# Kernel tuning notes

Measured on AMD Instinct MI355X. Metric: run time of the kernel, lower is better.

Reference implementation:

```python
import jax, jax.numpy as jnp
import numpy as np

B, C_LEN, Q_LEN, D = 8, 2048, 512, 1024


def setup_inputs() -> dict:
    key = jax.random.key(0)
    ks = jax.random.split(key, 10)
    scale = 1.0 / np.sqrt(D)
    return {
        "c": jax.random.normal(ks[0], (B, C_LEN, D), dtype=jnp.float32),
        "q": jax.random.normal(ks[1], (B, Q_LEN, D), dtype=jnp.float32),
        "w_cq": jax.random.normal(ks[2], (D,), dtype=jnp.float32) * scale,
        "b_cq": jax.random.normal(ks[3], (), dtype=jnp.float32) * scale,
        "w_c": jax.random.normal(ks[4], (D,), dtype=jnp.float32) * scale,
        "b_c": jax.random.normal(ks[5], (), dtype=jnp.float32) * scale,
        "w_q": jax.random.normal(ks[6], (D,), dtype=jnp.float32) * scale,
        "b_q": jax.random.normal(ks[7], (), dtype=jnp.float32) * scale,
        "W_l": jax.random.normal(ks[8], (D, 4 * D), dtype=jnp.float32) * (1.0 / np.sqrt(4 * D)),
        "b_l": jax.random.normal(ks[9], (D,), dtype=jnp.float32) * (1.0 / np.sqrt(4 * D)),
    }


def reference(c, q, w_cq, b_cq, w_c, b_c, w_q, b_q, W_l, b_l):
    # trilinear term: the original loops over q positions computing
    # att_weight_cq(c * q_i); since that Linear is rank-1, this is one einsum.
    cq = jnp.einsum('bcd,bqd,d->bcq', c, q, w_cq) + b_cq        # [B, C, Q]
    s = (c @ w_c + b_c)[:, :, None] + (q @ w_q + b_q)[:, None, :] + cq
    a = jax.nn.softmax(s, axis=2)                               # c2q attention
    c2q_att = jnp.einsum('bcq,bqd->bcd', a, q)                  # [B, C, D]
    b_att = jax.nn.softmax(jnp.max(s, axis=2), axis=1)          # [B, C]
    q2c_att = jnp.einsum('bc,bcd->bd', b_att, c)[:, None, :]    # [B, 1, D]
    x = jnp.concatenate([c, c2q_att, c * c2q_att, c * q2c_att], axis=-1)
    z = x @ W_l.T + b_l                                         # [B, C, D]
    return z
```

## Files before the change

kernel.cpp:

```cpp
#include <hip/hip_runtime.h>

typedef unsigned short u16;
typedef __attribute__((ext_vector_type(4))) float floatx4;
typedef __attribute__((ext_vector_type(4))) unsigned short u16x4;
typedef __attribute__((ext_vector_type(8))) short short8;
typedef __attribute__((ext_vector_type(8))) __bf16 bf16x8;

#define B_SZ 8
#define C_LEN 2048
#define Q_LEN 512
#define D_DIM 1024
#define K4 (4 * D_DIM)

static __device__ __forceinline__ u16 f2bf(float f) {
    union { float f; unsigned int u; } v; v.f = f;
    unsigned int r = v.u + 0x7FFFu + ((v.u >> 16) & 1u);
    return (u16)(r >> 16);
}
static __device__ __forceinline__ float bf2f(u16 h) {
    union { unsigned int u; float f; } v; v.u = ((unsigned int)h) << 16;
    return v.f;
}

static __device__ __forceinline__ void async16(const void* g, void* l) {
    __builtin_amdgcn_global_load_lds(
        (const __attribute__((address_space(1))) unsigned int*)g,
        (__attribute__((address_space(3))) unsigned int*)(unsigned int)(unsigned long long)l,
        16, 0, 0);
}

__global__ __launch_bounds__(256) void prep_kernel(
    const float* __restrict__ c, const float* __restrict__ q,
    const float* __restrict__ w_cq, const float* __restrict__ w_c, const float* __restrict__ w_q,
    u16* __restrict__ cbf, u16* __restrict__ qwbf, u16* __restrict__ qT,
    float* __restrict__ rowterm, float* __restrict__ colterm, float* __restrict__ q2c) {
    int blk = blockIdx.x;
    int tid = threadIdx.x;
    if (blk < 4096) {
        int row = blk * 4 + (tid >> 6);
        int lane = tid & 63;
        const float* src = c + (size_t)row * D_DIM;
        u16* dst = cbf + (size_t)row * D_DIM;
        float s = 0.f;
        #pragma unroll
        for (int j = 0; j < 4; ++j) {
            int idx = j * 256 + lane * 4;
            floatx4 a = *(const floatx4*)(src + idx);
            floatx4 w = *(const floatx4*)(w_c + idx);
            s += a[0]*w[0] + a[1]*w[1] + a[2]*w[2] + a[3]*w[3];
            u16x4 o;
            #pragma unroll
            for (int e = 0; e < 4; ++e) o[e] = f2bf(a[e]);
            *(u16x4*)(dst + idx) = o;
        }
        for (int off = 32; off; off >>= 1) s += __shfl_down(s, off);
        if (lane == 0) rowterm[row] = s;
    } else if (blk < 5120) {
        int row = (blk - 4096) * 4 + (tid >> 6);
        int lane = tid & 63;
        const float* src = q + (size_t)row * D_DIM;
        u16* dst = qwbf + (size_t)row * D_DIM;
        float s = 0.f;
        #pragma unroll
        for (int j = 0; j < 4; ++j) {
            int idx = j * 256 + lane * 4;
            floatx4 a  = *(const floatx4*)(src + idx);
            floatx4 wc = *(const floatx4*)(w_cq + idx);
            floatx4 wq = *(const floatx4*)(w_q + idx);
            s += a[0]*wq[0] + a[1]*wq[1] + a[2]*wq[2] + a[3]*wq[3];
            u16x4 o;
            #pragma unroll
            for (int e = 0; e < 4; ++e) o[e] = f2bf(a[e] * wc[e]);
            *(u16x4*)(dst + idx) = o;
        }
        for (int off = 32; off; off >>= 1) s += __shfl_down(s, off);
        if (lane == 0) colterm[row] = s;
    } else if (blk < 9216) {
        __shared__ float tile[32][33];
        int t = blk - 5120;
        int q0 = (t & 15) * 32;
        int d0 = ((t >> 4) & 31) * 32;
        int b = t >> 9;
        int tx = tid & 31, ty = tid >> 5;
        const float* qb = q + (size_t)b * Q_LEN * D_DIM;
        #pragma unroll
        for (int j = 0; j < 4; ++j) {
            int row = ty + j * 8;
            tile[row][tx] = qb[(size_t)(q0 + row) * D_DIM + d0 + tx];
        }
        __syncthreads();
        u16* qTb = qT + (size_t)b * D_DIM * Q_LEN;
        #pragma unroll
        for (int j = 0; j < 4; ++j) {
            int row = ty + j * 8;
            qTb[(size_t)(d0 + row) * Q_LEN + q0 + tx] = f2bf(tile[tx][row]);
        }
    } else {
        int i = (blk - 9216) * 256 + tid;
        q2c[i] = 0.0f;
    }
}

__global__ __launch_bounds__(256) void wmerge_all(const float* __restrict__ W, const float* __restrict__ q2c,
                                                  u16* __restrict__ Wm, u16* __restrict__ Wbf) {
    int n = blockIdx.x;
    int k = threadIdx.x * 4;
    const float* wr = W + (size_t)n * K4;
    floatx4 w1 = *(const floatx4*)(wr + k);
    floatx4 w4 = *(const floatx4*)(wr + 3072 + k);
    #pragma unroll
    for (int p = 0; p < 2; ++p) {
        int kk = p * 1024 + k;
        floatx4 v = *(const floatx4*)(wr + 1024 + kk);
        u16x4 o;
        #pragma unroll
        for (int e = 0; e < 4; ++e) o[e] = f2bf(v[e]);
        *(u16x4*)(Wbf + (size_t)n * 2048 + kk) = o;
    }
    #pragma unroll
    for (int b = 0; b < 8; ++b) {
        floatx4 g = *(const floatx4*)(q2c + (size_t)b * D_DIM + k);
        u16x4 o;
        #pragma unroll
        for (int e = 0; e < 4; ++e) o[e] = f2bf(w1[e] + w4[e] * g[e]);
        *(u16x4*)(Wm + (size_t)b * 1048576 + (size_t)n * 1024 + k) = o;
    }
}

template<int MODE>
__global__ __launch_bounds__(256) void gemm_async(
    const u16* __restrict__ A0, const u16* __restrict__ A1, const u16* __restrict__ A2,
    const u16* __restrict__ B0, const u16* __restrict__ B1,
    float* __restrict__ of, u16* __restrict__ ob, const float* __restrict__ bias) {
    constexpr int NSEC = (MODE == 2) ? 3 : 1;
    constexpr int KSEC = (MODE == 1) ? 512 : 1024;
    constexpr int LDO  = (MODE == 0) ? 512 : 1024;
    constexpr int NTILES = (MODE == 0) ? 4 : 8;
    __shared__ u16 As[128 * 64];
    __shared__ u16 Bs[128 * 64];
    const int tid  = threadIdx.x;
    const int lane = tid & 63;
    const int wave = tid >> 6;
    const int lin  = blockIdx.x;
    const int b    = lin & 7;
    const int rem  = lin >> 3;
    const int n0   = (rem % NTILES) * 128;
    const int m0   = (rem / NTILES) * 128;

    const u16* Aarr[NSEC];
    const u16* Barr[NSEC];
    int lda_[NSEC], ldb_[NSEC];
    if constexpr (MODE == 0) {
        Aarr[0] = A0 + (size_t)b * C_LEN * D_DIM; lda_[0] = 1024;
        Barr[0] = B0 + (size_t)b * Q_LEN * D_DIM; ldb_[0] = 1024;
    } else if constexpr (MODE == 1) {
        Aarr[0] = A0 + (size_t)b * C_LEN * Q_LEN; lda_[0] = 512;
        Barr[0] = B0 + (size_t)b * D_DIM * Q_LEN; ldb_[0] = 512;
    } else {
        Aarr[0] = A0 + (size_t)b * C_LEN * D_DIM;  lda_[0] = 1024;
        Barr[0] = B0 + (size_t)b * D_DIM * D_DIM;  ldb_[0] = 1024;
        Aarr[1] = A1 + (size_t)b * C_LEN * 2048;        lda_[1] = 2048;
        Barr[1] = B1;                                   ldb_[1] = 2048;
        Aarr[2] = A1 + (size_t)b * C_LEN * 2048 + 1024; lda_[2] = 2048;
        Barr[2] = B1 + 1024;                            ldb_[2] = 2048;
    }

    const int srow = lane >> 3;
    const int ssc  = ((lane & 7) ^ srow) * 8;

    floatx4 acc[4][4];
    #pragma unroll
    for (int i = 0; i < 4; ++i)
        #pragma unroll
        for (int j = 0; j < 4; ++j)
            acc[i][j] = (floatx4)(0.0f);

    const int wrow = (wave >> 1) * 64;
    const int wcol = (wave & 1) * 64;
    const int quad = lane >> 4;
    const int lrow = lane & 15;
    const int sw7  = lane & 7;

    #pragma unroll
    for (int sec = 0; sec < NSEC; ++sec) {
        const u16* __restrict__ Ab = Aarr[sec];
        const u16* __restrict__ Bb = Barr[sec];
        const int LA = lda_[sec];
        const int LB = ldb_[sec];
        for (int k0 = 0; k0 < KSEC; k0 += 64) {
            #pragma unroll
            for (int cc = 0; cc < 4; ++cc) {
                int ch = wave * 4 + cc;
                int rr = ch * 8 + srow;
                async16(Ab + (size_t)(m0 + rr) * LA + k0 + ssc, &As[ch * 512]);
            }
            #pragma unroll
            for (int cc = 0; cc < 4; ++cc) {
                int ch = wave * 4 + cc;
                int rr = ch * 8 + srow;
                async16(Bb + (size_t)(n0 + rr) * LB + k0 + ssc, &Bs[ch * 512]);
            }
            __syncthreads();
            #pragma unroll
            for (int h = 0; h < 2; ++h) {
                const int pc = ((h * 4 + quad) ^ sw7) * 8;
                bf16x8 af[4], bfr[4];
                #pragma unroll
                for (int i = 0; i < 4; ++i)
                    af[i] = __builtin_bit_cast(bf16x8, *(const short8*)&As[(wrow + i*16 + lrow) * 64 + pc]);
                #pragma unroll
                for (int j = 0; j < 4; ++j)
                    bfr[j] = __builtin_bit_cast(bf16x8, *(const short8*)&Bs[(wcol + j*16 + lrow) * 64 + pc]);
                #pragma unroll
                for (int i = 0; i < 4; ++i)
                    #pragma unroll
                    for (int j = 0; j < 4; ++j)
                        acc[i][j] = __builtin_amdgcn_mfma_f32_16x16x32_bf16(af[i], bfr[j], acc[i][j], 0, 0, 0);
            }
            __syncthreads();
        }
    }

    float* ofb = nullptr; u16* ccb = nullptr; const u16* cbr = nullptr;
    if (MODE == 0)      ofb = of + (size_t)b * C_LEN * Q_LEN;
    else if (MODE == 1) { ccb = ob + (size_t)b * C_LEN * 2048; cbr = A1 + (size_t)b * C_LEN * D_DIM; }
    else                ofb = of + (size_t)b * C_LEN * D_DIM;
    #pragma unroll
    for (int i = 0; i < 4; ++i) {
        #pragma unroll
        for (int j = 0; j < 4; ++j) {
            #pragma unroll
            for (int e = 0; e < 4; ++e) {
                int gm = m0 + wrow + i * 16 + quad * 4 + e;
                int gn = n0 + wcol + j * 16 + lrow;
                float v = acc[i][j][e];
                if (MODE == 0)      ofb[(size_t)gm * LDO + gn] = v;
                else if (MODE == 1) {
                    u16 p = f2bf(v);
                    float cv = bf2f(cbr[(size_t)gm * 1024 + gn]);
                    ccb[(size_t)gm * 2048 + gn]        = p;
                    ccb[(size_t)gm * 2048 + 1024 + gn] = f2bf(cv * bf2f(p));
                }
                else                ofb[(size_t)gm * LDO + gn] = v + bias[gn];
            }
        }
    }
}

__global__ void softmax_kernel(const float* __restrict__ S, const float* __restrict__ colterm,
                               u16* __restrict__ P, float* __restrict__ mbuf) {
    int row = blockIdx.x * 4 + (threadIdx.x >> 6);
    int lane = threadIdx.x & 63;
    int b = row >> 11;
    const float* sp = S + (size_t)row * Q_LEN;
    const float* cp = colterm + (size_t)b * Q_LEN;
    float v[8];
    float m = -1e30f;
    #pragma unroll
    for (int j = 0; j < 8; ++j) {
        int idx = j * 64 + lane;
        v[j] = sp[idx] + cp[idx];
        m = fmaxf(m, v[j]);
    }
    for (int off = 32; off; off >>= 1) m = fmaxf(m, __shfl_xor(m, off));
    float s = 0.f;
    #pragma unroll
    for (int j = 0; j < 8; ++j) { v[j] = __expf(v[j] - m); s += v[j]; }
    for (int off = 32; off; off >>= 1) s += __shfl_xor(s, off);
    float inv = 1.0f / s;
    u16* pp = P + (size_t)row * Q_LEN;
    #pragma unroll
    for (int j = 0; j < 8; ++j) pp[j * 64 + lane] = f2bf(v[j] * inv);
    if (lane == 0) mbuf[row] = m;
}

__global__ __launch_bounds__(256) void batt_kernel(const float* __restrict__ mbuf,
                                                   const float* __restrict__ rowterm,
                                                   float* __restrict__ batt) {
    __shared__ float red[8];
    int b = blockIdx.x;
    int tid = threadIdx.x;
    const float* mb = mbuf + (size_t)b * C_LEN;
    const float* rt = rowterm + (size_t)b * C_LEN;
    float v[8];
    float m = -1e30f;
    #pragma unroll
    for (int j = 0; j < 8; ++j) { int idx = j * 256 + tid; v[j] = mb[idx] + rt[idx]; m = fmaxf(m, v[j]); }
    for (int off = 32; off; off >>= 1) m = fmaxf(m, __shfl_xor(m, off));
    int wave = tid >> 6, lane = tid & 63;
    if (lane == 0) red[wave] = m;
    __syncthreads();
    m = fmaxf(fmaxf(red[0], red[1]), fmaxf(red[2], red[3]));
    float s = 0.f;
    #pragma unroll
    for (int j = 0; j < 8; ++j) { v[j] = __expf(v[j] - m); s += v[j]; }
    for (int off = 32; off; off >>= 1) s += __shfl_xor(s, off);
    if (lane == 0) red[4 + wave] = s;
    __syncthreads();
    s = red[4] + red[5] + red[6] + red[7];
    float inv = 1.0f / s;
    float* bb = batt + (size_t)b * C_LEN;
    #pragma unroll
    for (int j = 0; j < 8; ++j) bb[j * 256 + tid] = v[j] * inv;
}

__global__ __launch_bounds__(256) void q2c_kernel(const float* __restrict__ batt,
                                                  const u16* __restrict__ cbf,
                                                  float* __restrict__ q2c) {
    int d  = blockIdx.x * 256 + threadIdx.x;
    int b  = blockIdx.y;
    int c0 = blockIdx.z * 256;
    const u16* cb = cbf + ((size_t)b * C_LEN + c0) * D_DIM + d;
    const float* bb = batt + (size_t)b * C_LEN + c0;
    float s = 0.f;
    #pragma unroll 4
    for (int i = 0; i < 256; ++i) s += bb[i] * bf2f(cb[(size_t)i * D_DIM]);
    atomicAdd(&q2c[(size_t)b * D_DIM + d], s);
}

extern "C" void kernel_launch(void* const* d_in, const int* in_sizes, int n_in,
                              void* d_out, int out_size, void* d_ws, size_t ws_size,
                              hipStream_t stream) {
    const float* c   = (const float*)d_in[0];
    const float* q   = (const float*)d_in[1];
    const float* wcq = (const float*)d_in[2];
    const float* w_c = (const float*)d_in[4];
    const float* w_q = (const float*)d_in[6];
    const float* W_l = (const float*)d_in[8];
    const float* b_l = (const float*)d_in[9];
    float* out = (float*)d_out;

    char* ws = (char*)d_ws;
    u16*   cbf     = (u16*)ws;
    float* S       = (float*)(ws + 33554432);
    u16*   CC      = (u16*)(ws + 33554432);
    u16*   qwbf    = (u16*)(ws + 67108864);
    u16*   P       = (u16*)(ws + 100663296);
    u16*   Wm      = (u16*)(ws + 100663296);
    u16*   qT      = (u16*)(ws + 117440512);
    u16*   Wbf     = (u16*)(ws + 117440512);
    float* rowterm = (float*)(ws + 125829120);
    float* colterm = (float*)(ws + 125894656);
    float* mbuf    = (float*)(ws + 125911040);
    float* batt    = (float*)(ws + 125976576);
    float* q2c     = (float*)(ws + 126042112);

    prep_kernel<<<dim3(9248), dim3(256), 0, stream>>>(c, q, wcq, w_c, w_q,
                                                      cbf, qwbf, qT, rowterm, colterm, q2c);
    gemm_async<0><<<dim3(512), dim3(256), 0, stream>>>(cbf, nullptr, nullptr, qwbf, nullptr, S, nullptr, nullptr);
    softmax_kernel<<<dim3(4096), dim3(256), 0, stream>>>(S, colterm, P, mbuf);
    batt_kernel<<<dim3(8), dim3(256), 0, stream>>>(mbuf, rowterm, batt);
    q2c_kernel<<<dim3(4, 8, 8), dim3(256), 0, stream>>>(batt, cbf, q2c);
    gemm_async<1><<<dim3(1024), dim3(256), 0, stream>>>(P, cbf, nullptr, qT, nullptr, nullptr, CC, nullptr);
    wmerge_all<<<dim3(1024), dim3(256), 0, stream>>>(W_l, q2c, Wm, Wbf);
    gemm_async<2><<<dim3(1024), dim3(256), 0, stream>>>(cbf, CC, nullptr, Wm, Wbf, out, nullptr, b_l);
}
```

Before: 364.8 us.

## Reassociate c2q projection through W2 so final GEMM consumes P directly

The c2q_att @ W2^T term is rewritten as P @ (q @ W2^T), so a new small GEMM (mode 3) computes W2q = W2·q^T per batch and the final GEMM uses P (K=512) in place of the c2q block (K=1024). The mode-1 GEMM now only writes the c*c2q product instead of both c2q and the product. This shrinks the final GEMM's K, its A reads and mode-1's writes, at the cost of one extra GEMM that converts fp32 q to bf16 on the fly with synchronous loads. The reassociation also changes where bf16 rounding happens.

```diff
diff --git a/kernel.cpp b/kernel.cpp
--- a/kernel.cpp
+++ b/kernel.cpp
@@ -130,12 +130,12 @@
 template<int MODE>
 __global__ __launch_bounds__(256) void gemm_async(
     const u16* __restrict__ A0, const u16* __restrict__ A1, const u16* __restrict__ A2,
-    const u16* __restrict__ B0, const u16* __restrict__ B1,
+    const u16* __restrict__ B0, const u16* __restrict__ B1, const u16* __restrict__ B2,
+    const float* __restrict__ fB,
     float* __restrict__ of, u16* __restrict__ ob, const float* __restrict__ bias) {
     constexpr int NSEC = (MODE == 2) ? 3 : 1;
-    constexpr int KSEC = (MODE == 1) ? 512 : 1024;
-    constexpr int LDO  = (MODE == 0) ? 512 : 1024;
-    constexpr int NTILES = (MODE == 0) ? 4 : 8;
+    constexpr int LDO  = (MODE == 0 || MODE == 3) ? 512 : 1024;
+    constexpr int NTILES = (MODE == 0 || MODE == 3) ? 4 : 8;
     __shared__ u16 As[128 * 64];
     __shared__ u16 Bs[128 * 64];
     const int tid  = threadIdx.x;
@@ -149,20 +149,25 @@
 
     const u16* Aarr[NSEC];
     const u16* Barr[NSEC];
-    int lda_[NSEC], ldb_[NSEC];
+    const float* Bf = nullptr;
+    int lda_[NSEC], ldb_[NSEC], ks_[NSEC];
     if constexpr (MODE == 0) {
         Aarr[0] = A0 + (size_t)b * C_LEN * D_DIM; lda_[0] = 1024;
-        Barr[0] = B0 + (size_t)b * Q_LEN * D_DIM; ldb_[0] = 1024;
+        Barr[0] = B0 + (size_t)b * Q_LEN * D_DIM; ldb_[0] = 1024; ks_[0] = 1024;
     } else if constexpr (MODE == 1) {
         Aarr[0] = A0 + (size_t)b * C_LEN * Q_LEN; lda_[0] = 512;
-        Barr[0] = B0 + (size_t)b * D_DIM * Q_LEN; ldb_[0] = 512;
+        Barr[0] = B0 + (size_t)b * D_DIM * Q_LEN; ldb_[0] = 512;  ks_[0] = 512;
+    } else if constexpr (MODE == 3) {
+        Aarr[0] = A0;                             lda_[0] = 2048;
+        Barr[0] = nullptr;                        ldb_[0] = 1024;  ks_[0] = 1024;
+        Bf = fB + (size_t)b * Q_LEN * D_DIM;
     } else {
-        Aarr[0] = A0 + (size_t)b * C_LEN * D_DIM;  lda_[0] = 1024;
-        Barr[0] = B0 + (size_t)b * D_DIM * D_DIM;  ldb_[0] = 1024;
-        Aarr[1] = A1 + (size_t)b * C_LEN * 2048;        lda_[1] = 2048;
-        Barr[1] = B1;                                   ldb_[1] = 2048;
-        Aarr[2] = A1 + (size_t)b * C_LEN * 2048 + 1024; lda_[2] = 2048;
-        Barr[2] = B1 + 1024;                            ldb_[2] = 2048;
+        Aarr[0] = A0 + (size_t)b * C_LEN * D_DIM; lda_[0] = 1024;
+        Barr[0] = B0 + (size_t)b * D_DIM * D_DIM; ldb_[0] = 1024;  ks_[0] = 1024;
+        Aarr[1] = A1 + (size_t)b * C_LEN * Q_LEN; lda_[1] = 512;
+        Barr[1] = B1 + (size_t)b * D_DIM * Q_LEN; ldb_[1] = 512;   ks_[1] = 512;
+        Aarr[2] = A2 + (size_t)b * C_LEN * D_DIM; lda_[2] = 1024;
+        Barr[2] = B2 + 1024;                      ldb_[2] = 2048;  ks_[2] = 1024;
     }
 
     const int srow = lane >> 3;
@@ -187,18 +192,35 @@
         const u16* __restrict__ Bb = Barr[sec];
         const int LA = lda_[sec];
         const int LB = ldb_[sec];
-        for (int k0 = 0; k0 < KSEC; k0 += 64) {
+        const int KS = ks_[sec];
+        for (int k0 = 0; k0 < KS; k0 += 64) {
             #pragma unroll
             for (int cc = 0; cc < 4; ++cc) {
                 int ch = wave * 4 + cc;
                 int rr = ch * 8 + srow;
                 async16(Ab + (size_t)(m0 + rr) * LA + k0 + ssc, &As[ch * 512]);
             }
-            #pragma unroll
-            for (int cc = 0; cc < 4; ++cc) {
-                int ch = wave * 4 + cc;
-                int rr = ch * 8 + srow;
-                async16(Bb + (size_t)(n0 + rr) * LB + k0 + ssc, &Bs[ch * 512]);
+            if constexpr (MODE == 3) {
+                #pragma unroll
+                for (int cc = 0; cc < 4; ++cc) {
+                    int ch = wave * 4 + cc;
+                    int rr = ch * 8 + srow;
+                    const float* src = Bf + (size_t)(n0 + rr) * 1024 + k0 + ssc;
+                    floatx4 v0 = *(const floatx4*)src;
+                    floatx4 v1 = *(const floatx4*)(src + 4);
+                    u16x4 o0, o1;
+                    #pragma unroll
+                    for (int e = 0; e < 4; ++e) { o0[e] = f2bf(v0[e]); o1[e] = f2bf(v1[e]); }
+                    *(u16x4*)&Bs[ch * 512 + lane * 8]     = o0;
+                    *(u16x4*)&Bs[ch * 512 + lane * 8 + 4] = o1;
+                }
+            } else {
+                #pragma unroll
+                for (int cc = 0; cc < 4; ++cc) {
+                    int ch = wave * 4 + cc;
+                    int rr = ch * 8 + srow;
+                    async16(Bb + (size_t)(n0 + rr) * LB + k0 + ssc, &Bs[ch * 512]);
+                }
             }
             __syncthreads();
             #pragma unroll
@@ -221,10 +243,11 @@
         }
     }
 
-    float* ofb = nullptr; u16* ccb = nullptr; const u16* cbr = nullptr;
+    float* ofb = nullptr; u16* obb = nullptr; const u16* cbr = nullptr;
     if (MODE == 0)      ofb = of + (size_t)b * C_LEN * Q_LEN;
-    else if (MODE == 1) { ccb = ob + (size_t)b * C_LEN * 2048; cbr = A1 + (size_t)b * C_LEN * D_DIM; }
-    else                ofb = of + (size_t)b * C_LEN * D_DIM;
+    else if (MODE == 1) { obb = ob + (size_t)b * C_LEN * D_DIM; cbr = A1 + (size_t)b * C_LEN * D_DIM; }
+    else if (MODE == 2) ofb = of + (size_t)b * C_LEN * D_DIM;
+    else                obb = ob + (size_t)b * D_DIM * Q_LEN;
     #pragma unroll
     for (int i = 0; i < 4; ++i) {
         #pragma unroll
@@ -236,12 +259,11 @@
                 float v = acc[i][j][e];
                 if (MODE == 0)      ofb[(size_t)gm * LDO + gn] = v;
                 else if (MODE == 1) {
-                    u16 p = f2bf(v);
                     float cv = bf2f(cbr[(size_t)gm * 1024 + gn]);
-                    ccb[(size_t)gm * 2048 + gn]        = p;
-                    ccb[(size_t)gm * 2048 + 1024 + gn] = f2bf(cv * bf2f(p));
+                    obb[(size_t)gm * LDO + gn] = f2bf(cv * v);
                 }
-                else                ofb[(size_t)gm * LDO + gn] = v + bias[gn];
+                else if (MODE == 2) ofb[(size_t)gm * LDO + gn] = v + bias[gn];
+                else                obb[(size_t)gm * LDO + gn] = f2bf(v);
             }
         }
     }
@@ -333,25 +355,31 @@
     char* ws = (char*)d_ws;
     u16*   cbf     = (u16*)ws;
     float* S       = (float*)(ws + 33554432);
-    u16*   CC      = (u16*)(ws + 33554432);
+    u16*   cc2q    = (u16*)(ws + 33554432);
     u16*   qwbf    = (u16*)(ws + 67108864);
-    u16*   P       = (u16*)(ws + 100663296);
+    u16*   W2q     = (u16*)(ws + 67108864);
+    u16*   P       = (u16*)(ws + 75497472);
+    u16*   qT      = (u16*)(ws + 92274688);
     u16*   Wm      = (u16*)(ws + 100663296);
-    u16*   qT      = (u16*)(ws + 117440512);
     u16*   Wbf     = (u16*)(ws + 117440512);
-    float* rowterm = (float*)(ws + 125829120);
-    float* colterm = (float*)(ws + 125894656);
-    float* mbuf    = (float*)(ws + 125911040);
-    float* batt    = (float*)(ws + 125976576);
-    float* q2c     = (float*)(ws + 126042112);
+    float* rowterm = (float*)(ws + 121634816);
+    float* colterm = (float*)(ws + 121700352);
+    float* mbuf    = (float*)(ws + 121716736);
+    float* batt    = (float*)(ws + 121782272);
+    float* q2c     = (float*)(ws + 121847808);
 
     prep_kernel<<<dim3(9248), dim3(256), 0, stream>>>(c, q, wcq, w_c, w_q,
                                                       cbf, qwbf, qT, rowterm, colterm, q2c);
-    gemm_async<0><<<dim3(512), dim3(256), 0, stream>>>(cbf, nullptr, nullptr, qwbf, nullptr, S, nullptr, nullptr);
+    gemm_async<0><<<dim3(512), dim3(256), 0, stream>>>(cbf, nullptr, nullptr, qwbf, nullptr, nullptr,
+                                                       nullptr, S, nullptr, nullptr);
     softmax_kernel<<<dim3(4096), dim3(256), 0, stream>>>(S, colterm, P, mbuf);
     batt_kernel<<<dim3(8), dim3(256), 0, stream>>>(mbuf, rowterm, batt);
     q2c_kernel<<<dim3(4, 8, 8), dim3(256), 0, stream>>>(batt, cbf, q2c);
-    gemm_async<1><<<dim3(1024), dim3(256), 0, stream>>>(P, cbf, nullptr, qT, nullptr, nullptr, CC, nullptr);
     wmerge_all<<<dim3(1024), dim3(256), 0, stream>>>(W_l, q2c, Wm, Wbf);
-    gemm_async<2><<<dim3(1024), dim3(256), 0, stream>>>(cbf, CC, nullptr, Wm, Wbf, out, nullptr, b_l);
-}
+    gemm_async<3><<<dim3(256), dim3(256), 0, stream>>>(Wbf, nullptr, nullptr, nullptr, nullptr, nullptr,
+                                                       q, nullptr, W2q, nullptr);
+    gemm_async<1><<<dim3(1024), dim3(256), 0, stream>>>(P, cbf, nullptr, qT, nullptr, nullptr,
+                                                        nullptr, nullptr, cc2q, nullptr);
+    gemm_async<2><<<dim3(1024), dim3(256), 0, stream>>>(cbf, P, cc2q, Wm, W2q, Wbf,
+                                                        nullptr, out, nullptr, b_l);
+}
```

Result: no change. 365.9 us (+0.3%).
